# Performance work log

Hardware: AMD Instinct MI355X
Metric: run time of the kernel (lower is better)

## Reference

```python
import jax, jax.numpy as jnp
import numpy as np

N, E, D, L = 50000, 800000, 64, 4
ATOM_VOCAB, BOND_VOCAB, N_ATOM_F, N_BOND_F = 64, 8, 9, 3
BN_EPS = 1e-5


def _bn_train(z, g, b):
    # BatchNorm1d in training mode: batch mean, biased variance
    mu = jnp.mean(z, axis=0)
    var = jnp.mean((z - mu) ** 2, axis=0)
    return (z - mu) * jax.lax.rsqrt(var + BN_EPS) * g + b


def _multi_embed(tables, idx):
    # tables: [F, V, D], idx: [N, F] -> sum over F of tables[f][idx[:, f]] -> [N, D]
    return jax.vmap(lambda t, c: t[c], in_axes=(0, 1))(tables, idx).sum(0)


def setup_inputs() -> dict:
    key = jax.random.key(0)
    ks = jax.random.split(key, 8)
    s = 0.1
    return {
        "x": jax.random.randint(ks[0], (N, N_ATOM_F), 0, ATOM_VOCAB),
        "edge_index": jax.random.randint(ks[1], (2, E), 0, N),
        "edge_attr": jax.random.randint(ks[2], (E, N_BOND_F), 0, BOND_VOCAB),
        "atom_emb": jax.random.normal(ks[3], (N_ATOM_F, ATOM_VOCAB, D), jnp.float32) * s,
        "bond_emb": jax.random.normal(ks[4], (L, N_BOND_F, BOND_VOCAB, D), jnp.float32) * s,
        "lin1_w": jax.random.normal(ks[5], (L, D, 2 * D), jnp.float32) * s,
        "lin1_b": jnp.zeros((L, 2 * D), jnp.float32),
        "bn1_g": jnp.ones((L, 2 * D), jnp.float32),
        "bn1_b": jnp.zeros((L, 2 * D), jnp.float32),
        "lin2_w": jax.random.normal(ks[6], (L, 2 * D, D), jnp.float32) * s,
        "lin2_b": jnp.zeros((L, D), jnp.float32),
        "eps": jnp.zeros((L,), jnp.float32),
        "bn_g": jnp.ones((L, D), jnp.float32),
        "bn_b": jnp.zeros((L, D), jnp.float32),
    }


def reference(x, edge_index, edge_attr, atom_emb, bond_emb, lin1_w, lin1_b,
              bn1_g, bn1_b, lin2_w, lin2_b, eps, bn_g, bn_b):
    n_nodes = x.shape[0]
    n_layers = lin1_w.shape[0]
    src, dst = edge_index[0], edge_index[1]
    # AtomEncoder: sum of per-feature embeddings
    h = _multi_embed(atom_emb, x)  # [N, D]
    for l in range(n_layers):
        e = _multi_embed(bond_emb[l], edge_attr)  # [E, D] bond encoding
        msg = jax.nn.relu(h[src] + e)  # gather + elementwise message
        agg = jax.ops.segment_sum(msg, dst, num_segments=n_nodes)  # scatter-add
        z = (1.0 + eps[l]) * h + agg  # GIN update
        z = jax.nn.relu(_bn_train(z @ lin1_w[l] + lin1_b[l], bn1_g[l], bn1_b[l]))
        z = z @ lin2_w[l] + lin2_b[l]
        h = _bn_train(z, bn_g[l], bn_b[l])  # outer BatchNorm
        if l < n_layers - 1:
            h = jax.nn.relu(h)
    return h  # JK='last' node representation [N, D]
```

## Files before the change

### kernel.cpp

```cpp
#include <hip/hip_runtime.h>
#include <hip/hip_bf16.h>

#define NN 50000
#define NE 800000
#define NAF 9
#define NBF 3
#define BN_EPS 1e-5f
#define NBUK 196
#define CHUNK 8192
#define NTILE 3125
#define MMB 1563

typedef __attribute__((ext_vector_type(8))) short bf16x8;
typedef __attribute__((ext_vector_type(4))) float f32x4;

__device__ __forceinline__ short f2b(float f) {
  unsigned u = __float_as_uint(f);
  unsigned r = (u + 0x7FFFu + ((u >> 16) & 1u)) >> 16;
  return (short)r;
}

__device__ __forceinline__ bf16x8 pack8(float4 a, float4 b) {
  bf16x8 v;
  v[0] = f2b(a.x); v[1] = f2b(a.y); v[2] = f2b(a.z); v[3] = f2b(a.w);
  v[4] = f2b(b.x); v[5] = f2b(b.y); v[6] = f2b(b.z); v[7] = f2b(b.w);
  return v;
}

__global__ __launch_bounds__(256) void k_atom(const int* __restrict__ x,
                                              const float* __restrict__ aemb,
                                              float* __restrict__ h) {
  int node = (blockIdx.x * 256 + threadIdx.x) >> 6;
  int lane = threadIdx.x & 63;
  if (node >= NN) return;
  const int* xr = x + node * NAF;
  float acc = 0.f;
#pragma unroll
  for (int f = 0; f < NAF; ++f) acc += aemb[(f * 64 + xr[f]) * 64 + lane];
  h[(size_t)node * 64 + lane] = acc;
}

__global__ __launch_bounds__(256) void k_prep(const float* __restrict__ w1,
                                              const float* __restrict__ w2,
                                              bf16x8* __restrict__ pre1,
                                              bf16x8* __restrict__ pre2) {
  int f = (blockIdx.x & 15) * 256 + threadIdx.x;
  int lane = f & 63, c = lane & 15, g = lane >> 4;
  if (blockIdx.x < 16) {
    int kh = (f >> 6) & 1, t = (f >> 7) & 7, l = f >> 10;
    const float* w = w1 + (size_t)l * 64 * 128;
    bf16x8 v;
#pragma unroll
    for (int j = 0; j < 8; ++j) v[j] = f2b(w[(kh * 32 + g * 8 + j) * 128 + t * 16 + c]);
    pre1[f] = v;
  } else {
    int kf = (f >> 6) & 3, t = (f >> 8) & 3, l = f >> 10;
    const float* w = w2 + (size_t)l * 128 * 64;
    bf16x8 v;
#pragma unroll
    for (int j = 0; j < 8; ++j) v[j] = f2b(w[(kf * 32 + g * 8 + j) * 64 + t * 16 + c]);
    pre2[f] = v;
  }
}

__global__ __launch_bounds__(256) void k_red(const float* __restrict__ partial,
                                             float* __restrict__ st, int width) {
  int col = threadIdx.x;
  if (col >= width) return;
  int per = (MMB + gridDim.x - 1) / gridDim.x;
  int r0 = blockIdx.x * per;
  int r1 = min(MMB, r0 + per);
  float s = 0.f;
  int r = r0;
  for (; r + 4 <= r1; r += 4) {
    s += partial[(size_t)r * width + col] + partial[(size_t)(r + 1) * width + col]
       + partial[(size_t)(r + 2) * width + col] + partial[(size_t)(r + 3) * width + col];
  }
  for (; r < r1; ++r) s += partial[(size_t)r * width + col];
  atomicAdd(&st[col], s);
}

__global__ __launch_bounds__(1024) void k_pack_hist(const int* __restrict__ ei,
                                                    const int* __restrict__ ea,
                                                    uint2* __restrict__ pairs,
                                                    int* __restrict__ counts,
                                                    int* __restrict__ bcnt) {
  __shared__ int lh[NBUK];
  for (int i = threadIdx.x; i < NBUK; i += 1024) lh[i] = 0;
  __syncthreads();
  for (int e = blockIdx.x * 1024 + threadIdx.x; e < NE; e += gridDim.x * 1024) {
    int src = ei[e];
    int dst = ei[NE + e];
    unsigned code = (unsigned)(ea[e * 3] | (ea[e * 3 + 1] << 3) | (ea[e * 3 + 2] << 6));
    pairs[e] = make_uint2((unsigned)src | (code << 17), (unsigned)dst);
    atomicAdd(&counts[dst], 1);
    atomicAdd(&lh[dst >> 8], 1);
  }
  __syncthreads();
  for (int i = threadIdx.x; i < NBUK; i += 1024)
    if (lh[i]) atomicAdd(&bcnt[i], lh[i]);
}

__global__ __launch_bounds__(256) void k_scanb(const int* __restrict__ bcnt,
                                               int* __restrict__ bbase,
                                               int* __restrict__ bfill) {
  int tid = threadIdx.x;
  int c = (tid < NBUK) ? bcnt[tid] : 0;
  int lane = tid & 63, wid = tid >> 6;
  int inc = c;
#pragma unroll
  for (int off = 1; off < 64; off <<= 1) {
    int t = __shfl_up(inc, off);
    if (lane >= off) inc += t;
  }
  __shared__ int wt[4];
  if (lane == 63) wt[wid] = inc;
  __syncthreads();
  int woff = 0;
#pragma unroll
  for (int w = 0; w < 4; ++w) woff += (w < wid) ? wt[w] : 0;
  if (tid < NBUK) { int e = inc - c + woff; bbase[tid] = e; bfill[tid] = e; }
}

__global__ __launch_bounds__(256) void k_scan1(const int* __restrict__ counts,
                                               int* __restrict__ row_ptr,
                                               int* __restrict__ bsum) {
  int tid = threadIdx.x;
  int node = blockIdx.x * 256 + tid;
  int c = (node < NN) ? counts[node] : 0;
  int lane = tid & 63, wid = tid >> 6;
  int inc = c;
#pragma unroll
  for (int off = 1; off < 64; off <<= 1) {
    int t = __shfl_up(inc, off);
    if (lane >= off) inc += t;
  }
  __shared__ int wt[4];
  if (lane == 63) wt[wid] = inc;
  __syncthreads();
  int woff = 0;
#pragma unroll
  for (int w = 0; w < 4; ++w) woff += (w < wid) ? wt[w] : 0;
  if (node < NN) row_ptr[node] = inc - c + woff;
  if (tid == 255) bsum[blockIdx.x] = woff + inc;
}

__global__ __launch_bounds__(256) void k_scan2(const int* __restrict__ bsum,
                                               int* __restrict__ boff, int nb) {
  int tid = threadIdx.x;
  int c = (tid < nb) ? bsum[tid] : 0;
  int lane = tid & 63, wid = tid >> 6;
  int inc = c;
#pragma unroll
  for (int off = 1; off < 64; off <<= 1) {
    int t = __shfl_up(inc, off);
    if (lane >= off) inc += t;
  }
  __shared__ int wt[4];
  if (lane == 63) wt[wid] = inc;
  __syncthreads();
  int woff = 0;
#pragma unroll
  for (int w = 0; w < 4; ++w) woff += (w < wid) ? wt[w] : 0;
  if (tid < nb) boff[tid] = inc - c + woff;
}

__global__ __launch_bounds__(256) void k_scan3(int* __restrict__ row_ptr,
                                               const int* __restrict__ boff) {
  int node = blockIdx.x * 256 + threadIdx.x;
  if (node < NN) row_ptr[node] += boff[blockIdx.x];
  if (node == 0) row_ptr[NN] = NE;
}

__global__ __launch_bounds__(1024) void k_bin(const uint2* __restrict__ pairs,
                                              int* __restrict__ bfill,
                                              uint2* __restrict__ binned) {
  __shared__ uint2 st[CHUNK];
  __shared__ int lh[NBUK];
  __shared__ int gbase[NBUK];
  int tid = threadIdx.x;
  int base = blockIdx.x * CHUNK;
  int n = NE - base; if (n > CHUNK) n = CHUNK;
  for (int i = tid; i < NBUK; i += 1024) lh[i] = 0;
  __syncthreads();
  for (int i = tid; i < n; i += 1024) {
    uint2 p = pairs[base + i];
    st[i] = p;
    atomicAdd(&lh[p.y >> 8], 1);
  }
  __syncthreads();
  for (int i = tid; i < NBUK; i += 1024) {
    int c = lh[i];
    gbase[i] = c ? atomicAdd(&bfill[i], c) : 0;
  }
  __syncthreads();
  for (int i = tid; i < NBUK; i += 1024) lh[i] = 0;
  __syncthreads();
  for (int i = tid; i < n; i += 1024) {
    uint2 p = st[i];
    int b = p.y >> 8;
    int r = atomicAdd(&lh[b], 1);
    binned[gbase[b] + r] = p;
  }
}

__global__ __launch_bounds__(1024) void k_fin(const uint2* __restrict__ binned,
                                              const int* __restrict__ bbase,
                                              const int* __restrict__ bcnt,
                                              const int* __restrict__ row_ptr,
                                              unsigned* __restrict__ epack) {
  __shared__ int cur[256];
  int b = blockIdx.x;
  int tid = threadIdx.x;
  int node0 = b << 8;
  if (tid < 256) cur[tid] = (node0 + tid < NN) ? row_ptr[node0 + tid] : 0;
  __syncthreads();
  int s = bbase[b], n = bcnt[b];
  for (int i = tid; i < n; i += 1024) {
    uint2 p = binned[s + i];
    int pos = atomicAdd(&cur[p.y & 255], 1);
    epack[pos] = p.x;
  }
}

template <bool BN>
__device__ __forceinline__ void agg_body(const float* __restrict__ hin,
                                         const float* __restrict__ bemb,
                                         const float* __restrict__ eps, int l,
                                         const int* __restrict__ row_ptr,
                                         const unsigned* __restrict__ epack,
                                         const float* __restrict__ stp,
                                         const float* __restrict__ g,
                                         const float* __restrict__ bb,
                                         float* __restrict__ z) {
  __shared__ float tab[NBF * 8 * 64];
  __shared__ float nsb[128];
  const float* bt = bemb + (size_t)l * NBF * 8 * 64;
  for (int i = threadIdx.x; i < NBF * 8 * 64; i += 256) tab[i] = bt[i];
  if (BN && threadIdx.x < 64) {
    int c = threadIdx.x;
    const float inv = 1.0f / NN;
    float mu = stp[c] * inv;
    float var = stp[64 + c] * inv - mu * mu;
    float sc = rsqrtf(var + BN_EPS) * g[c];
    nsb[c] = sc;
    nsb[64 + c] = bb[c] - mu * sc;
  }
  __syncthreads();
  const float4* tab4 = (const float4*)tab;
  const float4* h4 = (const float4*)hin;

  int node = (blockIdx.x * 256 + threadIdx.x) >> 6;
  int lane = threadIdx.x & 63;
  if (node >= NN) return;
  int gr = lane >> 4;
  int c4 = lane & 15;
  float4 ns4 = {1.f, 1.f, 1.f, 1.f}, nb4 = {0.f, 0.f, 0.f, 0.f};
  if (BN) {
    ns4 = ((const float4*)nsb)[c4];
    nb4 = ((const float4*)(nsb + 64))[c4];
  }

  int beg = row_ptr[node], end = row_ptr[node + 1];
  float4 acc = {0.f, 0.f, 0.f, 0.f};

  auto edge = [&](unsigned p, float4 m) {
    unsigned cd = p >> 17;
    float4 ea_ = tab4[(cd & 7) * 16 + c4];
    float4 eb_ = tab4[128 + ((cd >> 3) & 7) * 16 + c4];
    float4 ec_ = tab4[256 + ((cd >> 6) & 7) * 16 + c4];
    if (BN) {
      m.x = fmaxf(fmaf(m.x, ns4.x, nb4.x), 0.f);
      m.y = fmaxf(fmaf(m.y, ns4.y, nb4.y), 0.f);
      m.z = fmaxf(fmaf(m.z, ns4.z, nb4.z), 0.f);
      m.w = fmaxf(fmaf(m.w, ns4.w, nb4.w), 0.f);
    }
    acc.x += fmaxf(m.x + ea_.x + eb_.x + ec_.x, 0.f);
    acc.y += fmaxf(m.y + ea_.y + eb_.y + ec_.y, 0.f);
    acc.z += fmaxf(m.z + ea_.z + eb_.z + ec_.z, 0.f);
    acc.w += fmaxf(m.w + ea_.w + eb_.w + ec_.w, 0.f);
  };

  int i = beg + gr;
  for (; i + 12 < end; i += 16) {
    unsigned p0 = epack[i];
    unsigned p1 = epack[i + 4];
    unsigned p2 = epack[i + 8];
    unsigned p3 = epack[i + 12];
    float4 m0 = h4[(size_t)(p0 & 0x1FFFFu) * 16 + c4];
    float4 m1 = h4[(size_t)(p1 & 0x1FFFFu) * 16 + c4];
    float4 m2 = h4[(size_t)(p2 & 0x1FFFFu) * 16 + c4];
    float4 m3 = h4[(size_t)(p3 & 0x1FFFFu) * 16 + c4];
    edge(p0, m0); edge(p1, m1); edge(p2, m2); edge(p3, m3);
  }
  for (; i < end; i += 4) {
    unsigned p0 = epack[i];
    float4 m0 = h4[(size_t)(p0 & 0x1FFFFu) * 16 + c4];
    edge(p0, m0);
  }
#pragma unroll
  for (int off = 16; off <= 32; off <<= 1) {
    acc.x += __shfl_xor(acc.x, off);
    acc.y += __shfl_xor(acc.y, off);
    acc.z += __shfl_xor(acc.z, off);
    acc.w += __shfl_xor(acc.w, off);
  }
  if (gr == 0) {
    float4 self = h4[(size_t)node * 16 + c4];
    if (BN) {
      self.x = fmaxf(fmaf(self.x, ns4.x, nb4.x), 0.f);
      self.y = fmaxf(fmaf(self.y, ns4.y, nb4.y), 0.f);
      self.z = fmaxf(fmaf(self.z, ns4.z, nb4.z), 0.f);
      self.w = fmaxf(fmaf(self.w, ns4.w, nb4.w), 0.f);
    }
    float se = 1.0f + eps[l];
    float4 out;
    out.x = fmaf(self.x, se, acc.x);
    out.y = fmaf(self.y, se, acc.y);
    out.z = fmaf(self.z, se, acc.z);
    out.w = fmaf(self.w, se, acc.w);
    ((float4*)z)[(size_t)node * 16 + c4] = out;
  }
}

__global__ __launch_bounds__(256) void k_agg0(const float* __restrict__ hin,
                                              const float* __restrict__ bemb,
                                              const float* __restrict__ eps, int l,
                                              const int* __restrict__ row_ptr,
                                              const unsigned* __restrict__ epack,
                                              float* __restrict__ z) {
  agg_body<false>(hin, bemb, eps, l, row_ptr, epack, nullptr, nullptr, nullptr, z);
}

__global__ __launch_bounds__(256) void k_aggbn(const float* __restrict__ hin,
                                               const float* __restrict__ bemb,
                                               const float* __restrict__ eps, int l,
                                               const int* __restrict__ row_ptr,
                                               const unsigned* __restrict__ epack,
                                               const float* __restrict__ stp,
                                               const float* __restrict__ g,
                                               const float* __restrict__ bb,
                                               float* __restrict__ z) {
  agg_body<true>(hin, bemb, eps, l, row_ptr, epack, stp, g, bb, z);
}

__global__ __launch_bounds__(256) void k_mm1(const float* __restrict__ z,
                                             const bf16x8* __restrict__ pre1,
                                             const float* __restrict__ b1,
                                             int l, float* __restrict__ y,
                                             float* __restrict__ part1) {
  __shared__ float lz[2][16 * 68];
  int tid = threadIdx.x;
  int lane = tid & 63;
  int wid = tid >> 6;
  int c = lane & 15;
  int g = lane >> 4;

  int t0 = blockIdx.x * 2;
  int ntl = (t0 + 1 < NTILE) ? 2 : 1;

  const float4* zt = (const float4*)(z + (size_t)t0 * 16 * 64);
  int nf4 = ntl * 256;
  for (int i = tid; i < nf4; i += 256) {
    float4 v = zt[i];
    int tile = i >> 8;
    int f4 = i & 255;
    int row = f4 >> 4, c4i = f4 & 15;
    *(float4*)(&lz[tile][row * 68 + c4i * 4]) = v;
  }

  bf16x8 Bf[2][2];
#pragma unroll
  for (int u = 0; u < 2; ++u)
#pragma unroll
    for (int kh = 0; kh < 2; ++kh)
      Bf[u][kh] = pre1[(((size_t)l * 8 + wid * 2 + u) * 2 + kh) * 64 + lane];
  float bias0 = b1[l * 128 + (wid * 2) * 16 + c];
  float bias1 = b1[l * 128 + (wid * 2 + 1) * 16 + c];

  __syncthreads();

  float ssum0 = 0.f, ssum1 = 0.f, sq0 = 0.f, sq1 = 0.f;

#pragma unroll
  for (int u = 0; u < 2; ++u) {
    if (u >= ntl) break;
    int rowbase = (t0 + u) * 16;
    const float* myz = lz[u];
    float4 q0 = *(const float4*)(myz + c * 68 + g * 8);
    float4 q1 = *(const float4*)(myz + c * 68 + g * 8 + 4);
    float4 q2 = *(const float4*)(myz + c * 68 + 32 + g * 8);
    float4 q3 = *(const float4*)(myz + c * 68 + 32 + g * 8 + 4);
    bf16x8 a0 = pack8(q0, q1);
    bf16x8 a1 = pack8(q2, q3);

    f32x4 acc0 = {bias0, bias0, bias0, bias0};
    acc0 = __builtin_amdgcn_mfma_f32_16x16x32_bf16(a0, Bf[0][0], acc0, 0, 0, 0);
    acc0 = __builtin_amdgcn_mfma_f32_16x16x32_bf16(a1, Bf[0][1], acc0, 0, 0, 0);
    f32x4 acc1 = {bias1, bias1, bias1, bias1};
    acc1 = __builtin_amdgcn_mfma_f32_16x16x32_bf16(a0, Bf[1][0], acc1, 0, 0, 0);
    acc1 = __builtin_amdgcn_mfma_f32_16x16x32_bf16(a1, Bf[1][1], acc1, 0, 0, 0);

    int tc0 = wid * 2, tc1 = wid * 2 + 1;
#pragma unroll
    for (int r = 0; r < 4; ++r) {
      float v0 = acc0[r], v1 = acc1[r];
      y[(size_t)(rowbase + g * 4 + r) * 128 + tc0 * 16 + c] = v0;
      y[(size_t)(rowbase + g * 4 + r) * 128 + tc1 * 16 + c] = v1;
      ssum0 += v0; sq0 = fmaf(v0, v0, sq0);
      ssum1 += v1; sq1 = fmaf(v1, v1, sq1);
    }
  }
  ssum0 += __shfl_xor(ssum0, 16); ssum0 += __shfl_xor(ssum0, 32);
  ssum1 += __shfl_xor(ssum1, 16); ssum1 += __shfl_xor(ssum1, 32);
  sq0 += __shfl_xor(sq0, 16); sq0 += __shfl_xor(sq0, 32);
  sq1 += __shfl_xor(sq1, 16); sq1 += __shfl_xor(sq1, 32);
  if (g == 0) {
    float* pp = part1 + (size_t)blockIdx.x * 256;
    pp[(wid * 2) * 16 + c] = ssum0;
    pp[(wid * 2 + 1) * 16 + c] = ssum1;
    pp[128 + (wid * 2) * 16 + c] = sq0;
    pp[128 + (wid * 2 + 1) * 16 + c] = sq1;
  }
}

__global__ __launch_bounds__(256) void k_mm2(const float* __restrict__ y,
                                             const bf16x8* __restrict__ pre2,
                                             const float* __restrict__ b2,
                                             const float* __restrict__ g1,
                                             const float* __restrict__ bb1,
                                             int l, float* __restrict__ z2,
                                             const float* __restrict__ st1,
                                             float* __restrict__ part2) {
  __shared__ float ly[2][16 * 132];
  __shared__ float ns[128], nb[128];
  int tid = threadIdx.x;
  int lane = tid & 63;
  int wid = tid >> 6;
  int c = lane & 15;
  int g = lane >> 4;

  int t0 = blockIdx.x * 2;
  int ntl = (t0 + 1 < NTILE) ? 2 : 1;

  const float4* yt = (const float4*)(y + (size_t)t0 * 16 * 128);
  int nf4 = ntl * 512;
  for (int i = tid; i < nf4; i += 256) {
    float4 v = yt[i];
    int tile = i >> 9;
    int f4 = i & 511;
    int row = f4 >> 5, c4i = f4 & 31;
    *(float4*)(&ly[tile][row * 132 + c4i * 4]) = v;
  }

  if (tid < 128) {
    int ch = tid;
    const float inv = 1.0f / NN;
    float mu = st1[ch] * inv;
    float var = st1[128 + ch] * inv - mu * mu;
    float sc = rsqrtf(var + BN_EPS) * g1[l * 128 + ch];
    ns[ch] = sc;
    nb[ch] = bb1[l * 128 + ch] - mu * sc;
  }

  bf16x8 Bf[4];
#pragma unroll
  for (int kf = 0; kf < 4; ++kf)
    Bf[kf] = pre2[(((size_t)l * 4 + wid) * 4 + kf) * 64 + lane];
  float bias = b2[l * 64 + wid * 16 + c];

  __syncthreads();

  const float4* nsf = (const float4*)ns;
  const float4* nbf = (const float4*)nb;
  float ssum = 0.f, sq = 0.f;

#pragma unroll
  for (int u = 0; u < 2; ++u) {
    if (u >= ntl) break;
    int rowbase = (t0 + u) * 16;
    const float* myy = ly[u];
    bf16x8 A[4];
#pragma unroll
    for (int kf = 0; kf < 4; ++kf) {
      float4 q0 = *(const float4*)(myy + c * 132 + kf * 32 + g * 8);
      float4 q1 = *(const float4*)(myy + c * 132 + kf * 32 + g * 8 + 4);
      float4 s0 = nsf[kf * 8 + g * 2];
      float4 s1 = nsf[kf * 8 + g * 2 + 1];
      float4 o0 = nbf[kf * 8 + g * 2];
      float4 o1 = nbf[kf * 8 + g * 2 + 1];
      float4 v0, v1;
      v0.x = fmaxf(fmaf(q0.x, s0.x, o0.x), 0.f);
      v0.y = fmaxf(fmaf(q0.y, s0.y, o0.y), 0.f);
      v0.z = fmaxf(fmaf(q0.z, s0.z, o0.z), 0.f);
      v0.w = fmaxf(fmaf(q0.w, s0.w, o0.w), 0.f);
      v1.x = fmaxf(fmaf(q1.x, s1.x, o1.x), 0.f);
      v1.y = fmaxf(fmaf(q1.y, s1.y, o1.y), 0.f);
      v1.z = fmaxf(fmaf(q1.z, s1.z, o1.z), 0.f);
      v1.w = fmaxf(fmaf(q1.w, s1.w, o1.w), 0.f);
      A[kf] = pack8(v0, v1);
    }
    f32x4 acc = {bias, bias, bias, bias};
#pragma unroll
    for (int kf = 0; kf < 4; ++kf)
      acc = __builtin_amdgcn_mfma_f32_16x16x32_bf16(A[kf], Bf[kf], acc, 0, 0, 0);
#pragma unroll
    for (int r = 0; r < 4; ++r) {
      float v = acc[r];
      z2[(size_t)(rowbase + g * 4 + r) * 64 + wid * 16 + c] = v;
      ssum += v; sq = fmaf(v, v, sq);
    }
  }
  ssum += __shfl_xor(ssum, 16); ssum += __shfl_xor(ssum, 32);
  sq += __shfl_xor(sq, 16); sq += __shfl_xor(sq, 32);
  if (g == 0) {
    float* pp = part2 + (size_t)blockIdx.x * 128;
    pp[wid * 16 + c] = ssum;
    pp[64 + wid * 16 + c] = sq;
  }
}

__global__ __launch_bounds__(256) void k_bn2(const float* __restrict__ z2,
                                             const float* __restrict__ g,
                                             const float* __restrict__ b,
                                             const float* __restrict__ st,
                                             float* __restrict__ h) {
  __shared__ float ns[64], nb[64];
  if (threadIdx.x < 64) {
    int c = threadIdx.x;
    const float inv = 1.0f / NN;
    float mu = st[c] * inv;
    float var = st[64 + c] * inv - mu * mu;
    float sc = rsqrtf(var + BN_EPS) * g[c];
    ns[c] = sc;
    nb[c] = b[c] - mu * sc;
  }
  __syncthreads();
  const float4* zin = (const float4*)z2;
  float4* hout = (float4*)h;
  int total = NN * 16;
  for (int i = blockIdx.x * 256 + threadIdx.x; i < total; i += gridDim.x * 256) {
    float4 v = zin[i];
    int c = (i & 15) * 4;
    v.x = fmaf(v.x, ns[c], nb[c]);
    v.y = fmaf(v.y, ns[c + 1], nb[c + 1]);
    v.z = fmaf(v.z, ns[c + 2], nb[c + 2]);
    v.w = fmaf(v.w, ns[c + 3], nb[c + 3]);
    hout[i] = v;
  }
}

extern "C" void kernel_launch(void* const* d_in, const int* in_sizes, int n_in,
                              void* d_out, int out_size, void* d_ws, size_t ws_size,
                              hipStream_t stream) {
  const int* x = (const int*)d_in[0];
  const int* ei = (const int*)d_in[1];
  const int* ea = (const int*)d_in[2];
  const float* aemb = (const float*)d_in[3];
  const float* bemb = (const float*)d_in[4];
  const float* l1w = (const float*)d_in[5];
  const float* l1b = (const float*)d_in[6];
  const float* g1 = (const float*)d_in[7];
  const float* bb1 = (const float*)d_in[8];
  const float* l2w = (const float*)d_in[9];
  const float* l2b = (const float*)d_in[10];
  const float* eps = (const float*)d_in[11];
  const float* bng = (const float*)d_in[12];
  const float* bnb = (const float*)d_in[13];
  float* out = (float*)d_out;

  char* p = (char*)d_ws;
  float* zA = (float*)p;           p += (size_t)NN * 64 * 4;
  float* y = (float*)p;            p += (size_t)NN * 128 * 4;
  float* zB = (float*)p;           p += (size_t)NN * 64 * 4;
  unsigned* epack = (unsigned*)p;  p += (size_t)NE * 4;
  int* row_ptr = (int*)p;          p += (size_t)(NN + 1) * 4;
  int* counts = (int*)p;           p += (size_t)NN * 4;
  int* bcnt = (int*)p;             p += 256 * 4;
  int* bbase = (int*)p;            p += 256 * 4;
  int* bfill = (int*)p;            p += 256 * 4;
  float* stats = (float*)p;        p += 4 * 384 * 4;
  int* bsum = (int*)p;             p += 256 * 4;
  int* boff = (int*)p;             p += 256 * 4;
  bf16x8* pre1 = (bf16x8*)p;       p += 4096 * 16;
  bf16x8* pre2 = (bf16x8*)p;       p += 4096 * 16;
  float* part1 = (float*)p;        p += (size_t)MMB * 256 * 4;
  float* part2 = (float*)p;        p += (size_t)MMB * 128 * 4;

  uint2* pairs = (uint2*)zA;
  uint2* binned = (uint2*)y;
  float* h0 = zB;

  const int NB = (NN + 255) / 256;

  hipMemsetAsync(counts, 0, (size_t)NN * 4, stream);
  hipMemsetAsync(bcnt, 0, 256 * 4, stream);
  hipMemsetAsync(stats, 0, 4 * 384 * 4, stream);

  k_prep<<<32, 256, 0, stream>>>(l1w, l2w, pre1, pre2);
  k_pack_hist<<<256, 1024, 0, stream>>>(ei, ea, pairs, counts, bcnt);
  k_scanb<<<1, 256, 0, stream>>>(bcnt, bbase, bfill);
  k_scan1<<<NB, 256, 0, stream>>>(counts, row_ptr, bsum);
  k_scan2<<<1, 256, 0, stream>>>(bsum, boff, NB);
  k_scan3<<<NB, 256, 0, stream>>>(row_ptr, boff);
  k_bin<<<(NE + CHUNK - 1) / CHUNK, 1024, 0, stream>>>(pairs, bfill, binned);
  k_fin<<<NBUK, 1024, 0, stream>>>(binned, bbase, bcnt, row_ptr, epack);

  k_atom<<<NN / 4, 256, 0, stream>>>(x, aemb, h0);

  for (int l = 0; l < 4; ++l) {
    float* st1 = stats + l * 384;
    float* st2 = st1 + 256;
    if (l == 0) {
      k_agg0<<<NN / 4, 256, 0, stream>>>(h0, bemb, eps, l, row_ptr, epack, zA);
    } else {
      const float* stp = stats + (l - 1) * 384 + 256;
      k_aggbn<<<NN / 4, 256, 0, stream>>>(zB, bemb, eps, l, row_ptr, epack,
                                          stp, bng + (l - 1) * 64, bnb + (l - 1) * 64, zA);
    }
    k_mm1<<<MMB, 256, 0, stream>>>(zA, pre1, l1b, l, y, part1);
    k_red<<<32, 256, 0, stream>>>(part1, st1, 256);
    k_mm2<<<MMB, 256, 0, stream>>>(y, pre2, l2b, g1, bb1, l, zB, st1, part2);
    k_red<<<32, 256, 0, stream>>>(part2, st2, 128);
  }
  k_bn2<<<1024, 256, 0, stream>>>(zB, bng + 3 * 64, bnb + 3 * 64,
                                  stats + 3 * 384 + 256, out);
}
```

Measured before the change: 409.2 us.

## Gather neighbor features from a bf16 copy prepared by a separate BN pass

Adds a k_hprep pass that applies the previous layer's batchnorm and ReLU once per node, writes the fp32 result back, and emits a bf16 copy of node features. The edge aggregation then gathers the half-width bf16 rows instead of fp32 rows and no longer recomputes BN per edge. This halves the bytes fetched by the random neighbor gather, which dominates aggregation traffic. In exchange it adds an extra full read and write pass per layer and loses precision in messages. The bf16 buffer aliases the y scratch buffer, which is safe only because y is rewritten by mm1 after aggregation.

After: 417.9 us. +2.1%, slower.

```diff
diff --git a/kernel.cpp b/kernel.cpp
--- a/kernel.cpp
+++ b/kernel.cpp
@@ -20,6 +20,10 @@
   return (short)r;
 }
 
+__device__ __forceinline__ float b2f(unsigned short v) {
+  return __uint_as_float(((unsigned)v) << 16);
+}
+
 __device__ __forceinline__ bf16x8 pack8(float4 a, float4 b) {
   bf16x8 v;
   v[0] = f2b(a.x); v[1] = f2b(a.y); v[2] = f2b(a.z); v[3] = f2b(a.w);
@@ -29,7 +33,8 @@
 
 __global__ __launch_bounds__(256) void k_atom(const int* __restrict__ x,
                                               const float* __restrict__ aemb,
-                                              float* __restrict__ h) {
+                                              float* __restrict__ h,
+                                              unsigned short* __restrict__ hb) {
   int node = (blockIdx.x * 256 + threadIdx.x) >> 6;
   int lane = threadIdx.x & 63;
   if (node >= NN) return;
@@ -38,6 +43,7 @@
 #pragma unroll
   for (int f = 0; f < NAF; ++f) acc += aemb[(f * 64 + xr[f]) * 64 + lane];
   h[(size_t)node * 64 + lane] = acc;
+  hb[(size_t)node * 64 + lane] = (unsigned short)f2b(acc);
 }
 
 __global__ __launch_bounds__(256) void k_prep(const float* __restrict__ w1,
@@ -80,6 +86,42 @@
   atomicAdd(&st[col], s);
 }
 
+__global__ __launch_bounds__(256) void k_hprep(float* __restrict__ zB,
+                                               const float* __restrict__ st,
+                                               const float* __restrict__ g,
+                                               const float* __restrict__ b,
+                                               unsigned short* __restrict__ hb) {
+  __shared__ float ns[64], nbv[64];
+  if (threadIdx.x < 64) {
+    int c = threadIdx.x;
+    const float inv = 1.0f / NN;
+    float mu = st[c] * inv;
+    float var = st[64 + c] * inv - mu * mu;
+    float sc = rsqrtf(var + BN_EPS) * g[c];
+    ns[c] = sc;
+    nbv[c] = b[c] - mu * sc;
+  }
+  __syncthreads();
+  float4* z4 = (float4*)zB;
+  ushort4* hb4 = (ushort4*)hb;
+  int total = NN * 16;
+  for (int i = blockIdx.x * 256 + threadIdx.x; i < total; i += gridDim.x * 256) {
+    float4 v = z4[i];
+    int c = (i & 15) * 4;
+    v.x = fmaxf(fmaf(v.x, ns[c], nbv[c]), 0.f);
+    v.y = fmaxf(fmaf(v.y, ns[c + 1], nbv[c + 1]), 0.f);
+    v.z = fmaxf(fmaf(v.z, ns[c + 2], nbv[c + 2]), 0.f);
+    v.w = fmaxf(fmaf(v.w, ns[c + 3], nbv[c + 3]), 0.f);
+    z4[i] = v;
+    ushort4 o;
+    o.x = (unsigned short)f2b(v.x);
+    o.y = (unsigned short)f2b(v.y);
+    o.z = (unsigned short)f2b(v.z);
+    o.w = (unsigned short)f2b(v.w);
+    hb4[i] = o;
+  }
+}
+
 __global__ __launch_bounds__(1024) void k_pack_hist(const int* __restrict__ ei,
                                                     const int* __restrict__ ea,
                                                     uint2* __restrict__ pairs,
@@ -223,62 +265,39 @@
   }
 }
 
-template <bool BN>
-__device__ __forceinline__ void agg_body(const float* __restrict__ hin,
-                                         const float* __restrict__ bemb,
-                                         const float* __restrict__ eps, int l,
-                                         const int* __restrict__ row_ptr,
-                                         const unsigned* __restrict__ epack,
-                                         const float* __restrict__ stp,
-                                         const float* __restrict__ g,
-                                         const float* __restrict__ bb,
-                                         float* __restrict__ z) {
+__global__ __launch_bounds__(256) void k_agg(const float* __restrict__ hf,
+                                             const unsigned short* __restrict__ hb,
+                                             const float* __restrict__ bemb,
+                                             const float* __restrict__ eps, int l,
+                                             const int* __restrict__ row_ptr,
+                                             const unsigned* __restrict__ epack,
+                                             float* __restrict__ z) {
   __shared__ float tab[NBF * 8 * 64];
-  __shared__ float nsb[128];
   const float* bt = bemb + (size_t)l * NBF * 8 * 64;
   for (int i = threadIdx.x; i < NBF * 8 * 64; i += 256) tab[i] = bt[i];
-  if (BN && threadIdx.x < 64) {
-    int c = threadIdx.x;
-    const float inv = 1.0f / NN;
-    float mu = stp[c] * inv;
-    float var = stp[64 + c] * inv - mu * mu;
-    float sc = rsqrtf(var + BN_EPS) * g[c];
-    nsb[c] = sc;
-    nsb[64 + c] = bb[c] - mu * sc;
-  }
   __syncthreads();
   const float4* tab4 = (const float4*)tab;
-  const float4* h4 = (const float4*)hin;
+  const ushort4* hb4 = (const ushort4*)hb;
+  const float4* hf4 = (const float4*)hf;
 
   int node = (blockIdx.x * 256 + threadIdx.x) >> 6;
   int lane = threadIdx.x & 63;
   if (node >= NN) return;
   int gr = lane >> 4;
   int c4 = lane & 15;
-  float4 ns4 = {1.f, 1.f, 1.f, 1.f}, nb4 = {0.f, 0.f, 0.f, 0.f};
-  if (BN) {
-    ns4 = ((const float4*)nsb)[c4];
-    nb4 = ((const float4*)(nsb + 64))[c4];
-  }
 
   int beg = row_ptr[node], end = row_ptr[node + 1];
   float4 acc = {0.f, 0.f, 0.f, 0.f};
 
-  auto edge = [&](unsigned p, float4 m) {
+  auto edge = [&](unsigned p, ushort4 hv) {
     unsigned cd = p >> 17;
     float4 ea_ = tab4[(cd & 7) * 16 + c4];
     float4 eb_ = tab4[128 + ((cd >> 3) & 7) * 16 + c4];
     float4 ec_ = tab4[256 + ((cd >> 6) & 7) * 16 + c4];
-    if (BN) {
-      m.x = fmaxf(fmaf(m.x, ns4.x, nb4.x), 0.f);
-      m.y = fmaxf(fmaf(m.y, ns4.y, nb4.y), 0.f);
-      m.z = fmaxf(fmaf(m.z, ns4.z, nb4.z), 0.f);
-      m.w = fmaxf(fmaf(m.w, ns4.w, nb4.w), 0.f);
-    }
-    acc.x += fmaxf(m.x + ea_.x + eb_.x + ec_.x, 0.f);
-    acc.y += fmaxf(m.y + ea_.y + eb_.y + ec_.y, 0.f);
-    acc.z += fmaxf(m.z + ea_.z + eb_.z + ec_.z, 0.f);
-    acc.w += fmaxf(m.w + ea_.w + eb_.w + ec_.w, 0.f);
+    acc.x += fmaxf(b2f(hv.x) + ea_.x + eb_.x + ec_.x, 0.f);
+    acc.y += fmaxf(b2f(hv.y) + ea_.y + eb_.y + ec_.y, 0.f);
+    acc.z += fmaxf(b2f(hv.z) + ea_.z + eb_.z + ec_.z, 0.f);
+    acc.w += fmaxf(b2f(hv.w) + ea_.w + eb_.w + ec_.w, 0.f);
   };
 
   int i = beg + gr;
@@ -287,16 +306,16 @@
     unsigned p1 = epack[i + 4];
     unsigned p2 = epack[i + 8];
     unsigned p3 = epack[i + 12];
-    float4 m0 = h4[(size_t)(p0 & 0x1FFFFu) * 16 + c4];
-    float4 m1 = h4[(size_t)(p1 & 0x1FFFFu) * 16 + c4];
-    float4 m2 = h4[(size_t)(p2 & 0x1FFFFu) * 16 + c4];
-    float4 m3 = h4[(size_t)(p3 & 0x1FFFFu) * 16 + c4];
-    edge(p0, m0); edge(p1, m1); edge(p2, m2); edge(p3, m3);
+    ushort4 h0 = hb4[(size_t)(p0 & 0x1FFFFu) * 16 + c4];
+    ushort4 h1 = hb4[(size_t)(p1 & 0x1FFFFu) * 16 + c4];
+    ushort4 h2 = hb4[(size_t)(p2 & 0x1FFFFu) * 16 + c4];
+    ushort4 h3 = hb4[(size_t)(p3 & 0x1FFFFu) * 16 + c4];
+    edge(p0, h0); edge(p1, h1); edge(p2, h2); edge(p3, h3);
   }
   for (; i < end; i += 4) {
     unsigned p0 = epack[i];
-    float4 m0 = h4[(size_t)(p0 & 0x1FFFFu) * 16 + c4];
-    edge(p0, m0);
+    ushort4 h0 = hb4[(size_t)(p0 & 0x1FFFFu) * 16 + c4];
+    edge(p0, h0);
   }
 #pragma unroll
   for (int off = 16; off <= 32; off <<= 1) {
@@ -306,13 +325,7 @@
     acc.w += __shfl_xor(acc.w, off);
   }
   if (gr == 0) {
-    float4 self = h4[(size_t)node * 16 + c4];
-    if (BN) {
-      self.x = fmaxf(fmaf(self.x, ns4.x, nb4.x), 0.f);
-      self.y = fmaxf(fmaf(self.y, ns4.y, nb4.y), 0.f);
-      self.z = fmaxf(fmaf(self.z, ns4.z, nb4.z), 0.f);
-      self.w = fmaxf(fmaf(self.w, ns4.w, nb4.w), 0.f);
-    }
+    float4 self = hf4[(size_t)node * 16 + c4];
     float se = 1.0f + eps[l];
     float4 out;
     out.x = fmaf(self.x, se, acc.x);
@@ -321,27 +334,6 @@
     out.w = fmaf(self.w, se, acc.w);
     ((float4*)z)[(size_t)node * 16 + c4] = out;
   }
-}
-
-__global__ __launch_bounds__(256) void k_agg0(const float* __restrict__ hin,
-                                              const float* __restrict__ bemb,
-                                              const float* __restrict__ eps, int l,
-                                              const int* __restrict__ row_ptr,
-                                              const unsigned* __restrict__ epack,
-                                              float* __restrict__ z) {
-  agg_body<false>(hin, bemb, eps, l, row_ptr, epack, nullptr, nullptr, nullptr, z);
-}
-
-__global__ __launch_bounds__(256) void k_aggbn(const float* __restrict__ hin,
-                                               const float* __restrict__ bemb,
-                                               const float* __restrict__ eps, int l,
-                                               const int* __restrict__ row_ptr,
-                                               const unsigned* __restrict__ epack,
-                                               const float* __restrict__ stp,
-                                               const float* __restrict__ g,
-                                               const float* __restrict__ bb,
-                                               float* __restrict__ z) {
-  agg_body<true>(hin, bemb, eps, l, row_ptr, epack, stp, g, bb, z);
 }
 
 __global__ __launch_bounds__(256) void k_mm1(const float* __restrict__ z,
@@ -589,6 +581,7 @@
 
   uint2* pairs = (uint2*)zA;
   uint2* binned = (uint2*)y;
+  unsigned short* hb = (unsigned short*)y;
   float* h0 = zB;
 
   const int NB = (NN + 255) / 256;
@@ -606,18 +599,17 @@
   k_bin<<<(NE + CHUNK - 1) / CHUNK, 1024, 0, stream>>>(pairs, bfill, binned);
   k_fin<<<NBUK, 1024, 0, stream>>>(binned, bbase, bcnt, row_ptr, epack);
 
-  k_atom<<<NN / 4, 256, 0, stream>>>(x, aemb, h0);
+  k_atom<<<NN / 4, 256, 0, stream>>>(x, aemb, h0, hb);
 
   for (int l = 0; l < 4; ++l) {
     float* st1 = stats + l * 384;
     float* st2 = st1 + 256;
-    if (l == 0) {
-      k_agg0<<<NN / 4, 256, 0, stream>>>(h0, bemb, eps, l, row_ptr, epack, zA);
-    } else {
+    if (l > 0) {
       const float* stp = stats + (l - 1) * 384 + 256;
-      k_aggbn<<<NN / 4, 256, 0, stream>>>(zB, bemb, eps, l, row_ptr, epack,
-                                          stp, bng + (l - 1) * 64, bnb + (l - 1) * 64, zA);
+      k_hprep<<<1024, 256, 0, stream>>>(zB, stp, bng + (l - 1) * 64,
+                                        bnb + (l - 1) * 64, hb);
     }
+    k_agg<<<NN / 4, 256, 0, stream>>>(zB, hb, bemb, eps, l, row_ptr, epack, zA);
     k_mm1<<<MMB, 256, 0, stream>>>(zA, pre1, l1b, l, y, part1);
     k_red<<<32, 256, 0, stream>>>(part1, st1, 256);
     k_mm2<<<MMB, 256, 0, stream>>>(y, pre2, l2b, g1, bb1, l, zB, st1, part2);
```
